# Kernel tuning notes

Hardware: AMD Instinct MI355X
Metric: run time of the kernel (lower is better)

The kernel has to match this reference:

```python
import jax, jax.numpy as jnp
import numpy as np

NL, H, PD, NH, NB = 4, 256, 64, 4, 65
B, L, AA = 2, 384, 48
DH = H // NH
MAX_REL = 32


def _ln(x, g, b):
    m = x.mean(-1, keepdims=True)
    v = ((x - m) ** 2).mean(-1, keepdims=True)
    return (x - m) * jax.lax.rsqrt(v + 1e-5) * g + b


def setup_inputs() -> dict:
    key = jax.random.key(0)
    ks = iter(jax.random.split(key, 64))
    w = lambda *s: jax.random.normal(next(ks), s, jnp.float32) * 0.02
    return dict(
        x=jax.random.normal(next(ks), (B, L, AA), jnp.float32),
        rp_w=w(AA, H), rp_b=jnp.zeros((H,), jnp.float32),
        pos_embed=w(L, H),
        pii_w=w(H, PD), pii_b=jnp.zeros((PD,), jnp.float32),
        pij_w=w(H, PD), pij_b=jnp.zeros((PD,), jnp.float32),
        rel_emb=w(2 * MAX_REL + 2, PD),
        ln_seq_g=jnp.ones((NL, H), jnp.float32), ln_seq_b=jnp.zeros((NL, H), jnp.float32),
        ln_pair_g=jnp.ones((NL, PD), jnp.float32), ln_pair_b=jnp.zeros((NL, PD), jnp.float32),
        pb_w=w(NL, PD, NH),
        in_w=w(NL, H, 3 * H), in_b=jnp.zeros((NL, 3 * H), jnp.float32),
        out_w=w(NL, H, H), out_b=jnp.zeros((NL, H), jnp.float32),
        ff_ln_g=jnp.ones((NL, H), jnp.float32), ff_ln_b=jnp.zeros((NL, H), jnp.float32),
        ff_w1=w(NL, H, 4 * H), ff_b1=jnp.zeros((NL, 4 * H), jnp.float32),
        ff_w2=w(NL, 4 * H, H), ff_b2=jnp.zeros((NL, H), jnp.float32),
        pu_ln_g=jnp.ones((NL, PD), jnp.float32), pu_ln_b=jnp.zeros((NL, PD), jnp.float32),
        pu_w1=w(NL, PD, PD), pu_b1=jnp.zeros((NL, PD), jnp.float32),
        pu_w2=w(NL, PD, PD), pu_b2=jnp.zeros((NL, PD), jnp.float32),
        outer_w=w(NL, 2 * H, PD), outer_b=jnp.zeros((NL, PD), jnp.float32),
        dh_ln_g=jnp.ones((PD,), jnp.float32), dh_ln_b=jnp.zeros((PD,), jnp.float32),
        dh_w1=w(PD, PD), dh_b1=jnp.zeros((PD,), jnp.float32),
        dh_w2=w(PD, NB), dh_b2=jnp.zeros((NB,), jnp.float32),
    )


def reference(x, rp_w, rp_b, pos_embed, pii_w, pii_b, pij_w, pij_b, rel_emb,
              ln_seq_g, ln_seq_b, ln_pair_g, ln_pair_b, pb_w, in_w, in_b,
              out_w, out_b, ff_ln_g, ff_ln_b, ff_w1, ff_b1, ff_w2, ff_b2,
              pu_ln_g, pu_ln_b, pu_w1, pu_b1, pu_w2, pu_b2, outer_w, outer_b,
              dh_ln_g, dh_ln_b, dh_w1, dh_b1, dh_w2, dh_b2):
    Bx, Lx, _ = x.shape
    gelu = lambda t: jax.nn.gelu(t, approximate=False)  # torch nn.GELU default (erf)
    h = x @ rp_w + rp_b + pos_embed[:Lx][None]
    # pair init: outer sum of two linear projections + clipped rel-pos embedding
    pair = (h @ pii_w + pii_b)[:, :, None, :] + (h @ pij_w + pij_b)[:, None, :, :]
    idx = jnp.arange(Lx)
    rel = jnp.clip(idx[None, :] - idx[:, None], -MAX_REL, MAX_REL) + MAX_REL  # (L,L)
    pair = pair + rel_emb[rel][None]
    for i in range(NL):
        seq_n = _ln(h, ln_seq_g[i], ln_seq_b[i])
        bias = _ln(pair, ln_pair_g[i], ln_pair_b[i]) @ pb_w[i]  # (B,L,L,NH)
        mask = bias.mean(axis=(0, 3))  # torch: permute->reshape(B*NH,L,L)->mean(0)
        qkv = seq_n @ in_w[i] + in_b[i]
        q, k, v = jnp.split(qkv, 3, axis=-1)
        q = q.reshape(Bx, Lx, NH, DH)
        k = k.reshape(Bx, Lx, NH, DH)
        v = v.reshape(Bx, Lx, NH, DH)
        scores = jnp.einsum('blhd,bmhd->bhlm', q, k) / float(np.sqrt(DH)) + mask
        attn = jax.nn.softmax(scores, axis=-1)
        o = jnp.einsum('bhlm,bmhd->blhd', attn, v).reshape(Bx, Lx, H)
        h = h + o @ out_w[i] + out_b[i]
        h = h + gelu(_ln(h, ff_ln_g[i], ff_ln_b[i]) @ ff_w1[i] + ff_b1[i]) @ ff_w2[i] + ff_b2[i]
        # outer_proj(cat([h_i, h_j])) == h@W[:H] outer-summed with h@W[H:]
        oi = h @ outer_w[i][:H]
        oj = h @ outer_w[i][H:]
        outer = oi[:, :, None, :] + oj[:, None, :, :] + outer_b[i]  # (B,L,L,PD)
        pair = pair + gelu(_ln(outer, pu_ln_g[i], pu_ln_b[i]) @ pu_w1[i] + pu_b1[i]) @ pu_w2[i] + pu_b2[i]
    logits = gelu(_ln(pair, dh_ln_g, dh_ln_b) @ dh_w1 + dh_b1) @ dh_w2 + dh_b2
    return (logits + jnp.swapaxes(logits, 1, 2)) / 2.0
```

## Files before the change

### kernel.cpp

```cpp
#include <hip/hip_runtime.h>
#include <math.h>

#define LSEQ 384
#define HD 256
#define PDIM 64
#define NHEAD 4
#define NBINS 65
#define BATCH 2
#define NTT (LSEQ / 16)
#define NTRI (NTT * (NTT + 1) / 2)

typedef __attribute__((ext_vector_type(8))) short bf16x8;
typedef __attribute__((ext_vector_type(16))) float f32x16;
typedef __attribute__((ext_vector_type(4))) float f32x4;
typedef __attribute__((ext_vector_type(4))) unsigned u32x4;
typedef __attribute__((ext_vector_type(4))) short s16x4;
#define MFMA32(a, b, c) __builtin_amdgcn_mfma_f32_32x32x16_bf16(a, b, c, 0, 0, 0)

template<int CTRL, int RMASK>
__device__ __forceinline__ float dpp_sum_step(float v) {
    int x = __builtin_amdgcn_update_dpp(0, __float_as_int(v), CTRL, RMASK, 0xf, true);
    return v + __int_as_float(x);
}
template<int CTRL, int RMASK>
// ... 81 lines not shown
                                        const unsigned short* __restrict__ srcB) {
    for (int idx = t; idx < 2048; idx += 256) {
        int rr2 = idx >> 5, cc2 = (idx & 31) * 2;
        *(unsigned*)&lw[0][rr2][cc2] = *(const unsigned*)(srcA + rr2 * 64 + cc2);
        *(unsigned*)&lw[1][rr2][cc2] = *(const unsigned*)(srcB + rr2 * 64 + cc2);
    }
}

__global__ void k_h_init(const float* __restrict__ x, const float* __restrict__ rp_w,
                         const float* __restrict__ rp_b, const float* __restrict__ pos,
                         float* __restrict__ h) {
    __shared__ float xs[48];
    int row = blockIdx.x;
    int l = row % LSEQ;
    int t = threadIdx.x;
    if (t < 48) xs[t] = x[row * 48 + t];
    __syncthreads();
    float acc = rp_b[t] + pos[l * HD + t];
#pragma unroll 8
    for (int a = 0; a < 48; ++a) acc += xs[a] * rp_w[a * HD + t];
    h[row * HD + t] = acc;
}

__global__ void k_proj2(const float* __restrict__ h, const float* __restrict__ wA,
                        const float* __restrict__ wB, const float* __restrict__ bA,
                        const float* __restrict__ bB, int center,
                        float* __restrict__ pA, float* __restrict__ pB) {
    __shared__ float hs[HD];
    int row = blockIdx.x;
    int t = threadIdx.x;
    hs[t] = h[row * HD + t];
    hs[t + 128] = h[row * HD + t + 128];
    __syncthreads();
    int col = t & 63;
    const float* w = (t < 64) ? wA : wB;
    const float* bias = (t < 64) ? bA : bB;
    float acc = bias ? bias[col] : 0.0f;
#pragma unroll 8
    for (int a = 0; a < HD; ++a) acc += hs[a] * w[a * PDIM + col];
    if (center) {
        float mean = wsum(acc) * (1.0f / PDIM);
        acc -= mean;
    }
    float* p = (t < 64) ? pA : pB;
    p[row * PDIM + col] = acc;
}

__global__ void __launch_bounds__(64) k_mask0(
    const float* __restrict__ pi, const float* __restrict__ pj,
    const float* __restrict__ rel_emb, const float* __restrict__ gpb,
    const float* __restrict__ cbv, float* __restrict__ mask_out) {
    __shared__ __align__(16) float pt[32][65];
    int blk = blockIdx.x;
    int row = blk / 12, seg = blk % 12;
    int b = row / LSEQ, i = row % LSEQ;
    int t = threadIdx.x;
    int pl = t & 31, hq = t >> 5;
    int j0 = seg * 32;
    float piv = pi[row * 64 + t];
    const float* pjb = pj + ((size_t)b * LSEQ + j0) * 64;
#pragma unroll 8
    for (int j = 0; j < 32; ++j) {
        int r = j0 + j - i; r = r < -32 ? -32 : (r > 32 ? 32 : r); r += 32;
        pt[j][t] = piv + pjb[j * 64 + t] + rel_emb[r * 64 + t];
    }
    __syncthreads();
    float vv[32];
    float sv = 0.0f;
#pragma unroll
    for (int c = 0; c < 32; ++c) { vv[c] = pt[pl][hq * 32 + c]; sv += vv[c]; }
    sv += __shfl_xor(sv, 32);
    float mean = sv * (1.0f / PDIM);
    float sd2 = 0.0f, sdg = 0.0f;
#pragma unroll
    for (int c = 0; c < 32; ++c) {
        float d = vv[c] - mean;
        sd2 = fmaf(d, d, sd2);
        sdg = fmaf(d, gpb[hq * 32 + c], sdg);
    }
    sd2 += __shfl_xor(sd2, 32);
    sdg += __shfl_xor(sdg, 32);
    float rsv = rsqrtf(sd2 * (1.0f / PDIM) + 1e-5f);
    float dot = rsv * sdg + cbv[0];
    if (hq == 0)
        atomicAdd(mask_out + i * LSEQ + j0 + pl, dot * (1.0f / (BATCH * NHEAD)));
}

__global__ void k_prep(const float* __restrict__ pu_ln_g, const float* __restrict__ pu_ln_b,
                       const float* __restrict__ pu_w1, const float* __restrict__ pu_b1,
                       const float* __restrict__ pu_w2,
                       const float* __restrict__ dh_ln_g, const float* __restrict__ dh_ln_b,
                       const float* __restrict__ dh_w1, const float* __restrict__ dh_b1,
                       const float* __restrict__ dh_w2,
                       unsigned short* __restrict__ w1hT, unsigned short* __restrict__ w1lT,
                       unsigned short* __restrict__ w2hT, unsigned short* __restrict__ w2lT,
                       float* __restrict__ b1p, float* __restrict__ w2c) {
    int i = blockIdx.x;
    int c = threadIdx.x;
    const float *g, *bb, *w1, *b1, *w2;
    int w2s;
    if (i < 4) { g = pu_ln_g + i * 64; bb = pu_ln_b + i * 64; w1 = pu_w1 + i * 4096;
                 b1 = pu_b1 + i * 64; w2 = pu_w2 + i * 4096; w2s = 64; }
    else       { g = dh_ln_g; bb = dh_ln_b; w1 = dh_w1; b1 = dh_b1; w2 = dh_w2; w2s = 65; }
    float accb = b1[c];
    for (int k = 0; k < 64; ++k) {
        float wv = w1[k * 64 + c];
        accb += bb[k] * wv;
        unsigned short h, l;
        split_bf(g[k] * wv, h, l);
        w1hT[i * 4096 + c * 64 + k] = h;
        w1lT[i * 4096 + c * 64 + k] = l;
        split_bf(w2[k * w2s + c], h, l);
        w2hT[i * 4096 + c * 64 + k] = h;
        w2lT[i * 4096 + c * 64 + k] = l;
    }
    b1p[i * 64 + c] = accb;
    if (i == 4) w2c[c] = dh_w2[c * 65 + 64];
}

__global__ void k_maskprep(const float* __restrict__ g, const float* __restrict__ bb,
                           const float* __restrict__ pbw, float* __restrict__ gp,
                           float* __restrict__ cb) {
    int li = blockIdx.x;
    int c = threadIdx.x;
    const float* pw = pbw + li * PDIM * NHEAD;
    float pbs = pw[c * 4] + pw[c * 4 + 1] + pw[c * 4 + 2] + pw[c * 4 + 3];
    gp[li * 64 + c] = g[li * 64 + c] * pbs;
    float s = wsum(bb[li * 64 + c] * pbs);
    if (c == 0) cb[li] = s;
}

__global__ void k_split_T(const float* __restrict__ src, unsigned short* __restrict__ dh,
                          unsigned short* __restrict__ dl, int K, int N,
                          int tiles_k, int tiles_n, size_t sstride, size_t dstride) {
    __shared__ float lds[64][65];
    int bid = blockIdx.x;
    int tpl = tiles_k * tiles_n;
    int layer = bid / tpl;
    int rest = bid % tpl;
    int kt = rest / tiles_n, nt = rest % tiles_n;
    const float* s = src + layer * sstride;
    int t = threadIdx.x, c = t & 63, r0 = t >> 6;
    for (int r = r0; r < 64; r += 4)
        lds[r][c] = s[(size_t)(kt * 64 + r) * N + nt * 64 + c];
    __syncthreads();
    unsigned short* oh = dh + layer * dstride;
    unsigned short* ol = dl + layer * dstride;
    for (int r = r0; r < 64; r += 4) {
        float v = lds[c][r];
        unsigned short h, l;
        split_bf(v, h, l);
        size_t o = (size_t)(nt * 64 + r) * K + kt * 64 + c;
        oh[o] = h;
        ol[o] = l;
    }
}

template<bool GELU>
__global__ void __launch_bounds__(64) k_gemm(
    const float* __restrict__ X, const unsigned short* __restrict__ wTh,
    const unsigned short* __restrict__ wTl, const float* __restrict__ bias,
    const float* __restrict__ R, float* __restrict__ OUT, int K, int N) {
    int idx = blockIdx.x;
    int lane = threadIdx.x & 63;
    int pl = lane & 31, hq = lane >> 5;
    int ntiles = N >> 5;
    int mt = idx / ntiles, nt = idx % ntiles;
    const float* xr = X + (size_t)(mt * 32 + pl) * K + 8 * hq;
    const unsigned short* bh = wTh + (size_t)(nt * 32 + pl) * K + 8 * hq;
    const unsigned short* bl = wTl + (size_t)(nt * 32 + pl) * K + 8 * hq;
    int n = nt * 32 + pl;
    float bv = bias[n];
    f32x16 acc;
#pragma unroll
    for (int r = 0; r < 16; ++r) {
        int mr = mt * 32 + (r & 3) + 8 * (r >> 2) + 4 * hq;
        acc[r] = bv + (R ? R[(size_t)mr * N + n] : 0.0f);
    }
#pragma unroll 4
    for (int s = 0; s < K; s += 16) {
        const f32x4* x4 = (const f32x4*)(xr + s);
        f32x4 xa = x4[0], xb = x4[1];
        float xv[8];
#pragma unroll
        for (int j = 0; j < 4; ++j) { xv[j] = xa[j]; xv[4 + j] = xb[j]; }
        u32x4 ah, al;
        pack8(xv, ah, al);
        bf16x8 bhv = *(const bf16x8*)(bh + s);
        bf16x8 blv = *(const bf16x8*)(bl + s);
        acc = MFMA32(as_bf(ah), bhv, acc);
        acc = MFMA32(as_bf(al), bhv, acc);
        acc = MFMA32(as_bf(ah), blv, acc);
    }
#pragma unroll
    for (int r = 0; r < 16; ++r) {
        int mr = mt * 32 + (r & 3) + 8 * (r >> 2) + 4 * hq;
        float v = acc[r];
        OUT[(size_t)mr * N + n] = GELU ? gelu_fast(v) : v;
    }
}

__global__ void k_ln_seq(const float* __restrict__ h, const float* __restrict__ g,
                         const float* __restrict__ b, float* __restrict__ out) {
    __shared__ float red[8];
    int row = blockIdx.x;
    int t = threadIdx.x;
    int w = t >> 6, lane = t & 63;
    float v = h[row * HD + t];
    float s = wsum(v);
    if (lane == 0) red[w] = s;
    __syncthreads();
    float mean = (red[0] + red[1] + red[2] + red[3]) * (1.0f / HD);
    float d = v - mean;
    float q = wsum(d * d);
    if (lane == 0) red[4 + w] = q;
    __syncthreads();
    float var = (red[4] + red[5] + red[6] + red[7]) * (1.0f / HD);
    out[row * HD + t] = d * rsqrtf(var + 1e-5f) * g[t] + b[t];
}

__global__ void k_attn(const float* __restrict__ qkv, const float* __restrict__ mask,
                       float* __restrict__ o) {
    __shared__ __align__(16) float qs[64];
    __shared__ float sc[LSEQ];
    __shared__ float red[8];
    __shared__ float op[4][64];
    int bid = blockIdx.x;
    int l = bid % LSEQ;
    int nh = (bid / LSEQ) & 3;
    int b = bid / (LSEQ * NHEAD);
    int t = threadIdx.x;
    int w = t >> 6, lane = t & 63;
    const float* qbase = qkv + ((size_t)(b * LSEQ + l)) * 768 + nh * 64;
    if (t < 64) qs[t] = qbase[t];
    __syncthreads();
    float lmax = -1e30f;
    float myv[2];
#pragma unroll
    for (int it = 0; it < 2; ++it) {
        int m = t + it * 256;
        if (m < LSEQ) {
            const float* kb = qkv + ((size_t)(b * LSEQ + m)) * 768 + 256 + nh * 64;
            const float4* k4 = (const float4*)kb;
            const float4* q4 = (const float4*)qs;
            float acc = 0.0f;
#pragma unroll
            for (int a = 0; a < 16; ++a) {
                float4 kv = k4[a], qv = q4[a];
                acc += qv.x * kv.x + qv.y * kv.y + qv.z * kv.z + qv.w * kv.w;
            }
            float s = acc * 0.125f + mask[l * LSEQ + m];
            myv[it] = s;
            lmax = fmaxf(lmax, s);
        } else myv[it] = -1e30f;
    }
    float wm = wmax(lmax);
    if (lane == 0) red[w] = wm;
    __syncthreads();
    float gmax = fmaxf(fmaxf(red[0], red[1]), fmaxf(red[2], red[3]));
    float lsum = 0.0f;
#pragma unroll
    for (int it = 0; it < 2; ++it) {
        int m = t + it * 256;
        if (m < LSEQ) {
            float e = expf(myv[it] - gmax);
            sc[m] = e;
            lsum += e;
        }
    }
    float ws = wsum(lsum);
    if (lane == 0) red[4 + w] = ws;
    __syncthreads();
    float inv = 1.0f / (red[4] + red[5] + red[6] + red[7]);
    int d = t & 63, gq = t >> 6;
    float part = 0.0f;
    for (int m = gq * 96; m < (gq + 1) * 96; ++m)
        part += sc[m] * qkv[((size_t)(b * LSEQ + m)) * 768 + 512 + nh * 64 + d];
    op[gq][d] = part;
    __syncthreads();
    if (t < 64) {
        float ov = (op[0][t] + op[1][t] + op[2][t] + op[3][t]) * inv;
        o[((size_t)(b * LSEQ + l)) * HD + nh * 64 + t] = ov;
    }
}

template<int MODE>
__global__ void __launch_bounds__(256, (MODE == 2) ? 2 : 3) k_pair_upd(
    const float* __restrict__ ojc,
    const float* __restrict__ oic,
    const unsigned short* __restrict__ w1hT, const unsigned short* __restrict__ w1lT,
    const float* __restrict__ b1p,
    const unsigned short* __restrict__ w2hT, const unsigned short* __restrict__ w2lT,
    const float* __restrict__ b2, float* __restrict__ pair,
    const float* __restrict__ gpb, const float* __restrict__ cbv,
    float* __restrict__ mask_out,
    const float* __restrict__ ipi, const float* __restrict__ ipj,
    const float* __restrict__ rel,
    const unsigned short* __restrict__ dw1h, const unsigned short* __restrict__ dw1l,
    const float* __restrict__ db1p,
    const unsigned short* __restrict__ dw2h, const unsigned short* __restrict__ dw2l,
    const float* __restrict__ w2c, const float* __restrict__ db2,
    float* __restrict__ outg) {
    constexpr bool DIST = (MODE == 2);
    __shared__ __align__(16) char smem[DIST ? 33344 : 17472];
    short (*lw)[64][68] = (short (*)[64][68])smem;
    int blk = blockIdx.x;
    int row = blk / 3, seg = blk % 3;
    int b = row / LSEQ;
    int t = threadIdx.x;
    int wave = t >> 6, lane = t & 63;
    int pl = lane & 31, hq = lane >> 5;
    int jj = wave * 32 + pl;
    int p = seg * 128 + jj;
    const float* ojr = ojc + ((size_t)b * LSEQ + p) * 64;
    const float* oir = oic + (size_t)row * 64;
    float* prp = pair + ((size_t)row * LSEQ + p) * 64;

    float v[32];
    {
        const f32x4* a4 = (const f32x4*)ojr;
        const f32x4* c4 = (const f32x4*)oir;
#pragma unroll
        for (int s = 0; s < 4; ++s) {
            f32x4 a = a4[4 * s + 2 * hq], aa = a4[4 * s + 2 * hq + 1];
            f32x4 c = c4[4 * s + 2 * hq], cc = c4[4 * s + 2 * hq + 1];
#pragma unroll
            for (int j = 0; j < 4; ++j) {
                v[8 * s + j] = a[j] + c[j];
                v[8 * s + 4 + j] = aa[j] + cc[j];
            }
        }
    }
    stage_w(lw, t, w1hT, w1lT);

    float ss = 0.0f;
#pragma unroll
    for (int i = 0; i < 32; ++i) ss = fmaf(v[i], v[i], ss);
    ss += __shfl_xor(ss, 32);
    float rs = rsqrtf(ss * (1.0f / PDIM) + 1e-5f);
#pragma unroll
    for (int i = 0; i < 32; ++i) v[i] *= rs;
    u32x4 zh[4], zl[4];
#pragma unroll
    for (int s = 0; s < 4; ++s) pack8(v + 8 * s, zh[s], zl[s]);

    const f32x4* b14 = (const f32x4*)b1p;
    f32x4 bi0[4], bi1[4];
#pragma unroll
    for (int g = 0; g < 4; ++g) { bi0[g] = b14[2 * g + hq]; bi1[g] = b14[8 + 2 * g + hq]; }

    __syncthreads();

    f32x16 acc0, acc1;
#pragma unroll
    for (int r = 0; r < 16; ++r) {
        acc0[r] = bi0[r >> 2][r & 3];
        acc1[r] = bi1[r >> 2][r & 3];
    }
#pragma unroll
    for (int s = 0; s < 4; ++s) {
        int ko = 16 * s + 8 * hq;
        bf16x8 a0h = ld8(&lw[0][pl][ko]);
        bf16x8 a0l = ld8(&lw[1][pl][ko]);
        bf16x8 a1h = ld8(&lw[0][32 + pl][ko]);
        bf16x8 a1l = ld8(&lw[1][32 + pl][ko]);
        bf16x8 zhs = as_bf(zh[s]), zls = as_bf(zl[s]);
        acc0 = MFMA32(a0h, zhs, acc0);
        acc0 = MFMA32(a0h, zls, acc0);
        acc0 = MFMA32(a0l, zhs, acc0);
        acc1 = MFMA32(a1h, zhs, acc1);
        acc1 = MFMA32(a1h, zls, acc1);
        acc1 = MFMA32(a1l, zhs, acc1);
    }
    __syncthreads();
    stage_w(lw, t, w2hT, w2lT);

    float u0[16], u1[16];
#pragma unroll
    for (int r = 0; r < 16; ++r) { u0[r] = gelu_erf(acc0[r]); u1[r] = gelu_erf(acc1[r]); }

    f32x4 r0[4], r1[4], q0[4], q1[4];
    {
        const f32x4* b24 = (const f32x4*)b2;
        if constexpr (MODE == 0) {
            int l = row % LSEQ;
            int rr_ = p - l; rr_ = rr_ < -32 ? -32 : (rr_ > 32 ? 32 : rr_); rr_ += 32;
            const f32x4* i4 = (const f32x4*)(ipi + (size_t)row * 64);
            const f32x4* j4 = (const f32x4*)(ipj + ((size_t)b * LSEQ + p) * 64);
            const f32x4* e4 = (const f32x4*)(rel + rr_ * 64);
#pragma unroll
            for (int g = 0; g < 4; ++g) {
                r0[g] = i4[2 * g + hq] + j4[2 * g + hq] + e4[2 * g + hq];
                r1[g] = i4[8 + 2 * g + hq] + j4[8 + 2 * g + hq] + e4[8 + 2 * g + hq];
                q0[g] = b24[2 * g + hq];
                q1[g] = b24[8 + 2 * g + hq];
            }
        } else {
            const f32x4* pr4 = (const f32x4*)prp;
#pragma unroll
            for (int g = 0; g < 4; ++g) {
                r0[g] = pr4[2 * g + hq];
                r1[g] = pr4[8 + 2 * g + hq];
                q0[g] = b24[2 * g + hq];
                q1[g] = b24[8 + 2 * g + hq];
            }
        }
    }

    float rA0[4], rB0[4], rA1[4], rB1[4];
#pragma unroll
    for (int i = 0; i < 4; ++i) {
        rA0[i] = __shfl_xor(hq ? u0[i] : u0[4 + i], 32);
        rB0[i] = __shfl_xor(hq ? u0[8 + i] : u0[12 + i], 32);
        rA1[i] = __shfl_xor(hq ? u1[i] : u1[4 + i], 32);
        rB1[i] = __shfl_xor(hq ? u1[8 + i] : u1[12 + i], 32);
    }
    u32x4 uh[4], ul[4];
#pragma unroll
    for (int s = 0; s < 4; ++s) {
        int tt = s >> 1, q = s & 1;
        float fg[8];
#pragma unroll
        for (int i = 0; i < 4; ++i) {
            float own_f = q ? (tt ? u1[8 + i] : u0[8 + i]) : (tt ? u1[i] : u0[i]);
            float own_s = q ? (tt ? u1[12 + i] : u0[12 + i]) : (tt ? u1[4 + i] : u0[4 + i]);
            float rcv   = q ? (tt ? rB1[i] : rB0[i]) : (tt ? rA1[i] : rA0[i]);
            fg[i]     = hq ? rcv : own_f;
            fg[4 + i] = hq ? own_s : rcv;
        }
        pack8(fg, uh[s], ul[s]);
    }

    __syncthreads();

    f32x16 c0, c1;
#pragma unroll
    for (int r = 0; r < 16; ++r) {
        int g = r >> 2, i = r & 3;
        c0[r] = q0[g][i] + r0[g][i];
        c1[r] = q1[g][i] + r1[g][i];
    }
#pragma unroll
    for (int s = 0; s < 4; ++s) {
        int ko = 16 * s + 8 * hq;
        bf16x8 a0h = ld8(&lw[0][pl][ko]);
        bf16x8 a0l = ld8(&lw[1][pl][ko]);
        bf16x8 a1h = ld8(&lw[0][32 + pl][ko]);
        bf16x8 a1l = ld8(&lw[1][32 + pl][ko]);
        bf16x8 uhs = as_bf(uh[s]), uls = as_bf(ul[s]);
        c0 = MFMA32(a0h, uhs, c0);
        c0 = MFMA32(a0h, uls, c0);
        c0 = MFMA32(a0l, uhs, c0);
        c1 = MFMA32(a1h, uhs, c1);
        c1 = MFMA32(a1h, uls, c1);
        c1 = MFMA32(a1l, uhs, c1);
    }

    if constexpr (!DIST) {
        const f32x4* gp4 = (const f32x4*)gpb;
        f32x4 gp0[4], gp1[4];
#pragma unroll
        for (int g = 0; g < 4; ++g) { gp0[g] = gp4[2 * g + hq]; gp1[g] = gp4[8 + 2 * g + hq]; }
        float sv = 0.0f;
#pragma unroll
        for (int r = 0; r < 16; ++r) sv += c0[r] + c1[r];
        sv += __shfl_xor(sv, 32);
        float mean = sv * (1.0f / PDIM);
        float sd2 = 0.0f, sdg = 0.0f;
#pragma unroll 4
        for (int r = 0; r < 16; ++r) {
            int g = r >> 2, i = r & 3;
            float d0 = c0[r] - mean, d1 = c1[r] - mean;
            sd2 = fmaf(d0, d0, sd2);
            sd2 = fmaf(d1, d1, sd2);
            sdg = fmaf(d0, gp0[g][i], sdg);
            sdg = fmaf(d1, gp1[g][i], sdg);
        }
        sd2 += __shfl_xor(sd2, 32);
        sdg += __shfl_xor(sdg, 32);
        float rsv = rsqrtf(sd2 * (1.0f / PDIM) + 1e-5f);
        float dot = rsv * sdg + cbv[0];
        if (hq == 0)
            atomicAdd(mask_out + (row % LSEQ) * LSEQ + p, dot * (1.0f / (BATCH * NHEAD)));
        f32x4* pw4 = (f32x4*)prp;
#pragma unroll
        for (int g = 0; g < 4; ++g) {
            f32x4 s0, s1;
#pragma unroll
            for (int i = 0; i < 4; ++i) { s0[i] = c0[4 * g + i]; s1[i] = c1[4 * g + i]; }
            pw4[2 * g + hq] = s0;
            pw4[8 + 2 * g + hq] = s1;
        }
    } else {
        float ra[4], rb[4], rc[4], rd[4];
#pragma unroll
        for (int i = 0; i < 4; ++i) {
            ra[i] = __shfl_xor(hq ? c0[i] : c0[4 + i], 32);
            rb[i] = __shfl_xor(hq ? c0[8 + i] : c0[12 + i], 32);
            rc[i] = __shfl_xor(hq ? c1[i] : c1[4 + i], 32);
            rd[i] = __shfl_xor(hq ? c1[8 + i] : c1[12 + i], 32);
        }
        float v2[32];
#pragma unroll
        for (int i = 0; i < 4; ++i) {
            v2[i]      = hq ? ra[i] : c0[i];
            v2[4 + i]  = hq ? c0[4 + i] : ra[i];
            v2[8 + i]  = hq ? rb[i] : c0[8 + i];
            v2[12 + i] = hq ? c0[12 + i] : rb[i];
            v2[16 + i] = hq ? rc[i] : c1[i];
            v2[20 + i] = hq ? c1[4 + i] : rc[i];
            v2[24 + i] = hq ? rd[i] : c1[8 + i];
            v2[28 + i] = hq ? c1[12 + i] : rd[i];
        }
        __syncthreads();
        stage_w(lw, t, dw1h, dw1l);

        float sm = 0.0f;
#pragma unroll
        for (int i = 0; i < 32; ++i) sm += v2[i];
        sm += __shfl_xor(sm, 32);
        float mean = sm * (1.0f / PDIM);
        float ss2 = 0.0f;
#pragma unroll
        for (int i = 0; i < 32; ++i) { v2[i] -= mean; ss2 = fmaf(v2[i], v2[i], ss2); }
        ss2 += __shfl_xor(ss2, 32);
        float rs2 = rsqrtf(ss2 * (1.0f / PDIM) + 1e-5f);
#pragma unroll
        for (int i = 0; i < 32; ++i) v2[i] *= rs2;
#pragma unroll
        for (int s = 0; s < 4; ++s) pack8(v2 + 8 * s, zh[s], zl[s]);

        const f32x4* d14 = (const f32x4*)db1p;
        const f32x4* d24 = (const f32x4*)db2;
        const f32x4* wc4 = (const f32x4*)w2c;
        f32x4 di0[4], di1[4], e0[4], e1[4], wc0[4], wc1[4];
#pragma unroll
        for (int g = 0; g < 4; ++g) {
            di0[g] = d14[2 * g + hq]; di1[g] = d14[8 + 2 * g + hq];
            e0[g] = d24[2 * g + hq];  e1[g] = d24[8 + 2 * g + hq];
            wc0[g] = wc4[2 * g + hq]; wc1[g] = wc4[8 + 2 * g + hq];
        }
        __syncthreads();

#pragma unroll
        for (int r = 0; r < 16; ++r) {
            acc0[r] = di0[r >> 2][r & 3];
            acc1[r] = di1[r >> 2][r & 3];
        }
#pragma unroll
        for (int s = 0; s < 4; ++s) {
            int ko = 16 * s + 8 * hq;
            bf16x8 a0h = ld8(&lw[0][pl][ko]);
            bf16x8 a0l = ld8(&lw[1][pl][ko]);
            bf16x8 a1h = ld8(&lw[0][32 + pl][ko]);
            bf16x8 a1l = ld8(&lw[1][32 + pl][ko]);
            bf16x8 zhs = as_bf(zh[s]), zls = as_bf(zl[s]);
            acc0 = MFMA32(a0h, zhs, acc0);
            acc0 = MFMA32(a0h, zls, acc0);
            acc0 = MFMA32(a0l, zhs, acc0);
            acc1 = MFMA32(a1h, zhs, acc1);
            acc1 = MFMA32(a1h, zls, acc1);
            acc1 = MFMA32(a1l, zhs, acc1);
        }
        __syncthreads();
        stage_w(lw, t, dw2h, dw2l);

        float p64 = 0.0f;
#pragma unroll
        for (int r = 0; r < 16; ++r) {
            int g = r >> 2, i = r & 3;
            u0[r] = gelu_erf(acc0[r]);
            u1[r] = gelu_erf(acc1[r]);
            p64 = fmaf(u0[r], wc0[g][i], p64);
            p64 = fmaf(u1[r], wc1[g][i], p64);
        }
        p64 += __shfl_xor(p64, 32);
#pragma unroll
        for (int i = 0; i < 4; ++i) {
            rA0[i] = __shfl_xor(hq ? u0[i] : u0[4 + i], 32);
            rB0[i] = __shfl_xor(hq ? u0[8 + i] : u0[12 + i], 32);
            rA1[i] = __shfl_xor(hq ? u1[i] : u1[4 + i], 32);
            rB1[i] = __shfl_xor(hq ? u1[8 + i] : u1[12 + i], 32);
        }
#pragma unroll
        for (int s = 0; s < 4; ++s) {
            int tt = s >> 1, q = s & 1;
            float fg[8];
#pragma unroll
            for (int i = 0; i < 4; ++i) {
                float own_f = q ? (tt ? u1[8 + i] : u0[8 + i]) : (tt ? u1[i] : u0[i]);
                float own_s = q ? (tt ? u1[12 + i] : u0[12 + i]) : (tt ? u1[4 + i] : u0[4 + i]);
                float rcv   = q ? (tt ? rB1[i] : rB0[i]) : (tt ? rA1[i] : rA0[i]);
                fg[i]     = hq ? rcv : own_f;
                fg[4 + i] = hq ? own_s : rcv;
            }
            pack8(fg, uh[s], ul[s]);
        }
        __syncthreads();

#pragma unroll
        for (int r = 0; r < 16; ++r) {
            c0[r] = e0[r >> 2][r & 3];
            c1[r] = e1[r >> 2][r & 3];
        }
#pragma unroll
        for (int s = 0; s < 4; ++s) {
            int ko = 16 * s + 8 * hq;
            bf16x8 a0h = ld8(&lw[0][pl][ko]);
            bf16x8 a0l = ld8(&lw[1][pl][ko]);
            bf16x8 a1h = ld8(&lw[0][32 + pl][ko]);
            bf16x8 a1l = ld8(&lw[1][32 + pl][ko]);
            bf16x8 uhs = as_bf(uh[s]), uls = as_bf(ul[s]);
            c0 = MFMA32(a0h, uhs, c0);
            c0 = MFMA32(a0h, uls, c0);
            c0 = MFMA32(a0l, uhs, c0);
            c1 = MFMA32(a1h, uhs, c1);
            c1 = MFMA32(a1h, uls, c1);
            c1 = MFMA32(a1l, uhs, c1);
        }
        __syncthreads();
        float (*pt)[65] = (float (*)[65])smem;
#pragma unroll
        for (int r = 0; r < 16; ++r) {
            int rr = (r & 3) + 8 * (r >> 2) + 4 * hq;
            pt[jj][rr] = c0[r];
            pt[jj][32 + rr] = c1[r];
        }
        if (hq == 0) pt[jj][64] = p64 + db2[64];
        __syncthreads();
        float4* dst = (float4*)(outg + ((size_t)row * LSEQ + seg * 128) * NBINS);
        const float4* srcl = (const float4*)&pt[0][0];
        for (int n = t; n < 128 * NBINS / 4; n += 256) dst[n] = srcl[n];
    }
}

__global__ void k_sym(float* __restrict__ out) {
    int u = blockIdx.x;
    int b = 0;
    if (u >= NTRI) { b = 1; u -= NTRI; }
    int lt = 0, rem = NTT;
    while (u >= rem) { u -= rem; ++lt; --rem; }
    int mt = lt + u;
    int t = threadIdx.x;
    int g = t >> 6, lane = t & 63;
    float* ob = out + (size_t)b * LSEQ * LSEQ * NBINS;
    for (int e = g; e < 256; e += 4) {
        int i = e >> 4, j = e & 15;
        if (lt == mt && j < i) continue;
        size_t ia = ((size_t)(lt * 16 + i) * LSEQ + (mt * 16 + j)) * NBINS;
        size_t ib = ((size_t)(mt * 16 + j) * LSEQ + (lt * 16 + i)) * NBINS;
        for (int k = lane; k < NBINS; k += 64) {
            float a = ob[ia + k], c = ob[ib + k];
            float vv = 0.5f * (a + c);
            ob[ia + k] = vv;
            if (ia != ib) ob[ib + k] = vv;
        }
    }
}

extern "C" void kernel_launch(void* const* d_in, const int* in_sizes, int n_in,
                              void* d_out, int out_size, void* d_ws, size_t ws_size,
                              hipStream_t stream) {
    const float* x        = (const float*)d_in[0];
    const float* rp_w     = (const float*)d_in[1];
    const float* rp_b     = (const float*)d_in[2];
    const float* pos      = (const float*)d_in[3];
    const float* pii_w    = (const float*)d_in[4];
    const float* pii_b    = (const float*)d_in[5];
    const float* pij_w    = (const float*)d_in[6];
    const float* pij_b    = (const float*)d_in[7];
    const float* rel_emb  = (const float*)d_in[8];
    const float* ln_seq_g = (const float*)d_in[9];
    const float* ln_seq_b = (const float*)d_in[10];
    const float* ln_pair_g= (const float*)d_in[11];
    const float* ln_pair_b= (const float*)d_in[12];
    const float* pb_w     = (const float*)d_in[13];
    const float* in_w     = (const float*)d_in[14];
    const float* in_b     = (const float*)d_in[15];
    const float* out_w    = (const float*)d_in[16];
    const float* out_b    = (const float*)d_in[17];
    const float* ff_ln_g  = (const float*)d_in[18];
    const float* ff_ln_b  = (const float*)d_in[19];
    const float* ff_w1    = (const float*)d_in[20];
    const float* ff_b1    = (const float*)d_in[21];
    const float* ff_w2    = (const float*)d_in[22];
    const float* ff_b2    = (const float*)d_in[23];
    const float* pu_ln_g  = (const float*)d_in[24];
    const float* pu_ln_b  = (const float*)d_in[25];
    const float* pu_w1    = (const float*)d_in[26];
    const float* pu_b1    = (const float*)d_in[27];
    const float* pu_w2    = (const float*)d_in[28];
    const float* pu_b2    = (const float*)d_in[29];
    const float* outer_w  = (const float*)d_in[30];
    const float* outer_b  = (const float*)d_in[31];
    const float* dh_ln_g  = (const float*)d_in[32];
    const float* dh_ln_b  = (const float*)d_in[33];
    const float* dh_w1    = (const float*)d_in[34];
    const float* dh_b1    = (const float*)d_in[35];
    const float* dh_w2    = (const float*)d_in[36];
    const float* dh_b2    = (const float*)d_in[37];
    float* outp = (float*)d_out;

    float* W = (float*)d_ws;
    float* h    = W;  W += BATCH * LSEQ * HD;
    float* sn   = W;  W += BATCH * LSEQ * HD;
    float* qkv  = W;  W += BATCH * LSEQ * 3 * HD;
    float* ob   = W;  W += BATCH * LSEQ * HD;
    float* mid  = W;  W += BATCH * LSEQ * 4 * HD;
    float* maskA= W;  W += LSEQ * LSEQ;
    float* maskB= W;  W += LSEQ * LSEQ;
    float* poi  = W;  W += BATCH * LSEQ * PDIM;
    float* poj  = W;  W += BATCH * LSEQ * PDIM;
    float* poi0 = W;  W += BATCH * LSEQ * PDIM;
    float* poj0 = W;  W += BATCH * LSEQ * PDIM;
    float* b1p  = W;  W += 5 * 64;
    float* w2c  = W;  W += 64;
    float* gpb  = W;  W += 4 * 64;
    float* cbv  = W;  W += 64;
    unsigned short* w1hT = (unsigned short*)W;  W += 5 * 2048;
    unsigned short* w1lT = (unsigned short*)W;  W += 5 * 2048;
    unsigned short* w2hT = (unsigned short*)W;  W += 5 * 2048;
    unsigned short* w2lT = (unsigned short*)W;  W += 5 * 2048;
    unsigned short* qwT_h = (unsigned short*)W;  W += 4 * 196608 / 2;
    unsigned short* qwT_l = (unsigned short*)W;  W += 4 * 196608 / 2;
    unsigned short* owT_h = (unsigned short*)W;  W += 4 * 65536 / 2;
    unsigned short* owT_l = (unsigned short*)W;  W += 4 * 65536 / 2;
    unsigned short* f1T_h = (unsigned short*)W;  W += 4 * 262144 / 2;
    unsigned short* f1T_l = (unsigned short*)W;  W += 4 * 262144 / 2;
    unsigned short* f2T_h = (unsigned short*)W;  W += 4 * 262144 / 2;
    unsigned short* f2T_l = (unsigned short*)W;  W += 4 * 262144 / 2;
    float* pair = W;  W += (size_t)BATCH * LSEQ * LSEQ * PDIM;

    const int rows = BATCH * LSEQ;

    k_prep<<<5, 64, 0, stream>>>(pu_ln_g, pu_ln_b, pu_w1, pu_b1, pu_w2,
                                 dh_ln_g, dh_ln_b, dh_w1, dh_b1, dh_w2,
                                 w1hT, w1lT, w2hT, w2lT, b1p, w2c);
    k_maskprep<<<4, 64, 0, stream>>>(ln_pair_g, ln_pair_b, pb_w, gpb, cbv);
    k_split_T<<<4 * 4 * 12, 256, 0, stream>>>(in_w,  qwT_h, qwT_l, 256, 768,  4, 12, 196608, 196608);
    k_split_T<<<4 * 4 * 4,  256, 0, stream>>>(out_w, owT_h, owT_l, 256, 256,  4, 4,  65536,  65536);
    k_split_T<<<4 * 4 * 16, 256, 0, stream>>>(ff_w1, f1T_h, f1T_l, 256, 1024, 4, 16, 262144, 262144);
    k_split_T<<<4 * 16 * 4, 256, 0, stream>>>(ff_w2, f2T_h, f2T_l, 1024, 256, 16, 4, 262144, 262144);
    k_h_init<<<rows, 256, 0, stream>>>(x, rp_w, rp_b, pos, h);
    k_proj2<<<rows, 128, 0, stream>>>(h, pii_w, pij_w, pii_b, pij_b, 0, poi0, poj0);
    hipMemsetAsync(maskA, 0, LSEQ * LSEQ * sizeof(float), stream);
    k_mask0<<<rows * 12, 64, 0, stream>>>(poi0, poj0, rel_emb, gpb, cbv, maskA);

    float* mcur = maskA;
    float* mnext = maskB;
    for (int i = 0; i < 4; ++i) {
        k_ln_seq<<<rows, 256, 0, stream>>>(h, ln_seq_g + i * HD, ln_seq_b + i * HD, sn);
        k_gemm<false><<<576, 64, 0, stream>>>(sn, qwT_h + i * 196608, qwT_l + i * 196608,
                                              in_b + i * 768, nullptr, qkv, 256, 768);
        k_attn<<<BATCH * NHEAD * LSEQ, 256, 0, stream>>>(qkv, mcur, ob);
        k_gemm<false><<<192, 64, 0, stream>>>(ob, owT_h + i * 65536, owT_l + i * 65536,
                                              out_b + i * 256, h, h, 256, 256);
        k_ln_seq<<<rows, 256, 0, stream>>>(h, ff_ln_g + i * HD, ff_ln_b + i * HD, sn);
        k_gemm<true><<<768, 64, 0, stream>>>(sn, f1T_h + i * 262144, f1T_l + i * 262144,
                                             ff_b1 + i * 1024, nullptr, mid, 256, 1024);
        k_gemm<false><<<192, 64, 0, stream>>>(mid, f2T_h + i * 262144, f2T_l + i * 262144,
                                              ff_b2 + i * 256, h, h, 1024, 256);
        k_proj2<<<rows, 128, 0, stream>>>(h, outer_w + i * 2 * HD * PDIM,
                                          outer_w + i * 2 * HD * PDIM + HD * PDIM,
                                          outer_b + i * PDIM, nullptr, 1, poi, poj);
        if (i == 0) {
            hipMemsetAsync(mnext, 0, LSEQ * LSEQ * sizeof(float), stream);
            k_pair_upd<0><<<rows * 3, 256, 0, stream>>>(
                poj, poi,
                w1hT, w1lT, b1p, w2hT, w2lT, pu_b2, pair,
                gpb + 64, cbv + 1, mnext, poi0, poj0, rel_emb,
                nullptr, nullptr, nullptr, nullptr, nullptr, nullptr, nullptr, nullptr);
            float* tmp = mcur; mcur = mnext; mnext = tmp;
        } else if (i < 3) {
            hipMemsetAsync(mnext, 0, LSEQ * LSEQ * sizeof(float), stream);
            k_pair_upd<1><<<rows * 3, 256, 0, stream>>>(
                poj, poi,
                w1hT + i * 4096, w1lT + i * 4096, b1p + i * 64,
                w2hT + i * 4096, w2lT + i * 4096, pu_b2 + i * PDIM, pair,
                gpb + (i + 1) * 64, cbv + (i + 1), mnext,
                nullptr, nullptr, nullptr,
                nullptr, nullptr, nullptr, nullptr, nullptr, nullptr, nullptr, nullptr);
            float* tmp = mcur; mcur = mnext; mnext = tmp;
        } else {
            k_pair_upd<2><<<rows * 3, 256, 0, stream>>>(
                poj, poi,
                w1hT + 3 * 4096, w1lT + 3 * 4096, b1p + 3 * 64,
                w2hT + 3 * 4096, w2lT + 3 * 4096, pu_b2 + 3 * PDIM, pair,
                nullptr, nullptr, nullptr,
                nullptr, nullptr, nullptr,
                w1hT + 4 * 4096, w1lT + 4 * 4096, b1p + 4 * 64,
                w2hT + 4 * 4096, w2lT + 4 * 4096, w2c, dh_b2, outp);
        }
    }

    k_sym<<<2 * NTRI, 256, 0, stream>>>(outp);
}
```

Baseline: 1.025 ms.

## Process full pair row per block with both MLP weights staged once

For the non-final pair-update modes, each block now handles a whole row (three 128-column segments in a loop) instead of one segment. Both weight matrices are staged into shared memory once, in separate buffers, before the loop. This removes the repeated weight staging and the intra-block syncs between the two GEMMs. In exchange the grid is one third the size and shared memory per block doubles, which may lower occupancy and parallelism.

```diff
diff --git a/kernel.cpp b/kernel.cpp
--- a/kernel.cpp
+++ b/kernel.cpp
@@ -407,100 +407,271 @@
     const float* __restrict__ w2c, const float* __restrict__ db2,
     float* __restrict__ outg) {
     constexpr bool DIST = (MODE == 2);
-    __shared__ __align__(16) char smem[DIST ? 33344 : 17472];
-    short (*lw)[64][68] = (short (*)[64][68])smem;
-    int blk = blockIdx.x;
-    int row = blk / 3, seg = blk % 3;
-    int b = row / LSEQ;
+    __shared__ __align__(16) char smem[DIST ? 33344 : 34816];
     int t = threadIdx.x;
     int wave = t >> 6, lane = t & 63;
     int pl = lane & 31, hq = lane >> 5;
     int jj = wave * 32 + pl;
-    int p = seg * 128 + jj;
-    const float* ojr = ojc + ((size_t)b * LSEQ + p) * 64;
-    const float* oir = oic + (size_t)row * 64;
-    float* prp = pair + ((size_t)row * LSEQ + p) * 64;
-
-    float v[32];
-    {
-        const f32x4* a4 = (const f32x4*)ojr;
-        const f32x4* c4 = (const f32x4*)oir;
+
+    if constexpr (!DIST) {
+        short (*lw1)[64][68] = (short (*)[64][68])smem;
+        short (*lw2)[64][68] = (short (*)[64][68])(smem + 17408);
+        int row = blockIdx.x;
+        int b = row / LSEQ;
+        int l = row % LSEQ;
+        const float* oir = oic + (size_t)row * 64;
+        stage_w(lw1, t, w1hT, w1lT);
+        stage_w(lw2, t, w2hT, w2lT);
+        __syncthreads();
+
+        for (int seg = 0; seg < 3; ++seg) {
+            int p = seg * 128 + jj;
+            const float* ojr = ojc + ((size_t)b * LSEQ + p) * 64;
+            float* prp = pair + ((size_t)row * LSEQ + p) * 64;
+
+            float v[32];
+            {
+                const f32x4* a4 = (const f32x4*)ojr;
+                const f32x4* c4 = (const f32x4*)oir;
+#pragma unroll
+                for (int s = 0; s < 4; ++s) {
+                    f32x4 a = a4[4 * s + 2 * hq], aa = a4[4 * s + 2 * hq + 1];
+                    f32x4 c = c4[4 * s + 2 * hq], cc = c4[4 * s + 2 * hq + 1];
+#pragma unroll
+                    for (int j = 0; j < 4; ++j) {
+                        v[8 * s + j] = a[j] + c[j];
+                        v[8 * s + 4 + j] = aa[j] + cc[j];
+                    }
+                }
+            }
+            float ss = 0.0f;
+#pragma unroll
+            for (int i = 0; i < 32; ++i) ss = fmaf(v[i], v[i], ss);
+            ss += __shfl_xor(ss, 32);
+            float rs = rsqrtf(ss * (1.0f / PDIM) + 1e-5f);
+#pragma unroll
+            for (int i = 0; i < 32; ++i) v[i] *= rs;
+            u32x4 zh[4], zl[4];
+#pragma unroll
+            for (int s = 0; s < 4; ++s) pack8(v + 8 * s, zh[s], zl[s]);
+
+            const f32x4* b14 = (const f32x4*)b1p;
+            f32x16 acc0, acc1;
+#pragma unroll
+            for (int g = 0; g < 4; ++g) {
+                f32x4 bb0 = b14[2 * g + hq], bb1 = b14[8 + 2 * g + hq];
+#pragma unroll
+                for (int i = 0; i < 4; ++i) {
+                    acc0[4 * g + i] = bb0[i];
+                    acc1[4 * g + i] = bb1[i];
+                }
+            }
+#pragma unroll
+            for (int s = 0; s < 4; ++s) {
+                int ko = 16 * s + 8 * hq;
+                bf16x8 a0h = ld8(&lw1[0][pl][ko]);
+                bf16x8 a0l = ld8(&lw1[1][pl][ko]);
+                bf16x8 a1h = ld8(&lw1[0][32 + pl][ko]);
+                bf16x8 a1l = ld8(&lw1[1][32 + pl][ko]);
+                bf16x8 zhs = as_bf(zh[s]), zls = as_bf(zl[s]);
+                acc0 = MFMA32(a0h, zhs, acc0);
+                acc0 = MFMA32(a0h, zls, acc0);
+                acc0 = MFMA32(a0l, zhs, acc0);
+                acc1 = MFMA32(a1h, zhs, acc1);
+                acc1 = MFMA32(a1h, zls, acc1);
+                acc1 = MFMA32(a1l, zhs, acc1);
+            }
+            float u0[16], u1[16];
+#pragma unroll
+            for (int r = 0; r < 16; ++r) { u0[r] = gelu_erf(acc0[r]); u1[r] = gelu_erf(acc1[r]); }
+
+            f32x4 r0[4], r1[4], q0[4], q1[4];
+            {
+                const f32x4* b24 = (const f32x4*)b2;
+                if constexpr (MODE == 0) {
+                    int rr_ = p - l; rr_ = rr_ < -32 ? -32 : (rr_ > 32 ? 32 : rr_); rr_ += 32;
+                    const f32x4* i4 = (const f32x4*)(ipi + (size_t)row * 64);
+                    const f32x4* j4 = (const f32x4*)(ipj + ((size_t)b * LSEQ + p) * 64);
+                    const f32x4* e4 = (const f32x4*)(rel + rr_ * 64);
+#pragma unroll
+                    for (int g = 0; g < 4; ++g) {
+                        r0[g] = i4[2 * g + hq] + j4[2 * g + hq] + e4[2 * g + hq];
+                        r1[g] = i4[8 + 2 * g + hq] + j4[8 + 2 * g + hq] + e4[8 + 2 * g + hq];
+                        q0[g] = b24[2 * g + hq];
+                        q1[g] = b24[8 + 2 * g + hq];
+                    }
+                } else {
+                    const f32x4* pr4 = (const f32x4*)prp;
+#pragma unroll
+                    for (int g = 0; g < 4; ++g) {
+                        r0[g] = pr4[2 * g + hq];
+                        r1[g] = pr4[8 + 2 * g + hq];
+                        q0[g] = b24[2 * g + hq];
+                        q1[g] = b24[8 + 2 * g + hq];
+                    }
+                }
+            }
+
+            float rA0[4], rB0[4], rA1[4], rB1[4];
+#pragma unroll
+            for (int i = 0; i < 4; ++i) {
+                rA0[i] = __shfl_xor(hq ? u0[i] : u0[4 + i], 32);
+                rB0[i] = __shfl_xor(hq ? u0[8 + i] : u0[12 + i], 32);
+                rA1[i] = __shfl_xor(hq ? u1[i] : u1[4 + i], 32);
+                rB1[i] = __shfl_xor(hq ? u1[8 + i] : u1[12 + i], 32);
+            }
+            u32x4 uh[4], ul[4];
+#pragma unroll
+            for (int s = 0; s < 4; ++s) {
+                int tt = s >> 1, q = s & 1;
+                float fg[8];
+#pragma unroll
+                for (int i = 0; i < 4; ++i) {
+                    float own_f = q ? (tt ? u1[8 + i] : u0[8 + i]) : (tt ? u1[i] : u0[i]);
+                    float own_s = q ? (tt ? u1[12 + i] : u0[12 + i]) : (tt ? u1[4 + i] : u0[4 + i]);
+                    float rcv   = q ? (tt ? rB1[i] : rB0[i]) : (tt ? rA1[i] : rA0[i]);
+                    fg[i]     = hq ? rcv : own_f;
+                    fg[4 + i] = hq ? own_s : rcv;
+                }
+                pack8(fg, uh[s], ul[s]);
+            }
+
+            f32x16 c0, c1;
+#pragma unroll
+            for (int r = 0; r < 16; ++r) {
+                int g = r >> 2, i = r & 3;
+                c0[r] = q0[g][i] + r0[g][i];
+                c1[r] = q1[g][i] + r1[g][i];
+            }
+#pragma unroll
+            for (int s = 0; s < 4; ++s) {
+                int ko = 16 * s + 8 * hq;
+                bf16x8 a0h = ld8(&lw2[0][pl][ko]);
+                bf16x8 a0l = ld8(&lw2[1][pl][ko]);
+                bf16x8 a1h = ld8(&lw2[0][32 + pl][ko]);
+                bf16x8 a1l = ld8(&lw2[1][32 + pl][ko]);
+                bf16x8 uhs = as_bf(uh[s]), uls = as_bf(ul[s]);
+                c0 = MFMA32(a0h, uhs, c0);
+                c0 = MFMA32(a0h, uls, c0);
+                c0 = MFMA32(a0l, uhs, c0);
+                c1 = MFMA32(a1h, uhs, c1);
+                c1 = MFMA32(a1h, uls, c1);
+                c1 = MFMA32(a1l, uhs, c1);
+            }
+
+            {
+                const f32x4* gp4 = (const f32x4*)gpb;
+                f32x4 gp0[4], gp1[4];
+#pragma unroll
+                for (int g = 0; g < 4; ++g) { gp0[g] = gp4[2 * g + hq]; gp1[g] = gp4[8 + 2 * g + hq]; }
+                float sv = 0.0f;
+#pragma unroll
+                for (int r = 0; r < 16; ++r) sv += c0[r] + c1[r];
+                sv += __shfl_xor(sv, 32);
+                float mean = sv * (1.0f / PDIM);
+                float sd2 = 0.0f, sdg = 0.0f;
+#pragma unroll 4
+                for (int r = 0; r < 16; ++r) {
+                    int g = r >> 2, i = r & 3;
+                    float d0 = c0[r] - mean, d1 = c1[r] - mean;
+                    sd2 = fmaf(d0, d0, sd2);
+                    sd2 = fmaf(d1, d1, sd2);
+                    sdg = fmaf(d0, gp0[g][i], sdg);
+                    sdg = fmaf(d1, gp1[g][i], sdg);
+                }
+                sd2 += __shfl_xor(sd2, 32);
+                sdg += __shfl_xor(sdg, 32);
+                float rsv = rsqrtf(sd2 * (1.0f / PDIM) + 1e-5f);
+                float dot = rsv * sdg + cbv[0];
+                if (hq == 0)
+                    atomicAdd(mask_out + l * LSEQ + p, dot * (1.0f / (BATCH * NHEAD)));
+            }
+            f32x4* pw4 = (f32x4*)prp;
+#pragma unroll
+            for (int g = 0; g < 4; ++g) {
+                f32x4 s0, s1;
+#pragma unroll
+                for (int i = 0; i < 4; ++i) { s0[i] = c0[4 * g + i]; s1[i] = c1[4 * g + i]; }
+                pw4[2 * g + hq] = s0;
+                pw4[8 + 2 * g + hq] = s1;
+            }
+        }
+    } else {
+        short (*lw)[64][68] = (short (*)[64][68])smem;
+        int blk = blockIdx.x;
+        int row = blk / 3, seg = blk % 3;
+        int b = row / LSEQ;
+        int p = seg * 128 + jj;
+        const float* ojr = ojc + ((size_t)b * LSEQ + p) * 64;
+        const float* oir = oic + (size_t)row * 64;
+        float* prp = pair + ((size_t)row * LSEQ + p) * 64;
+
+        float v[32];
+        {
+            const f32x4* a4 = (const f32x4*)ojr;
+            const f32x4* c4 = (const f32x4*)oir;
+#pragma unroll
+            for (int s = 0; s < 4; ++s) {
+                f32x4 a = a4[4 * s + 2 * hq], aa = a4[4 * s + 2 * hq + 1];
+                f32x4 c = c4[4 * s + 2 * hq], cc = c4[4 * s + 2 * hq + 1];
+#pragma unroll
+                for (int j = 0; j < 4; ++j) {
+                    v[8 * s + j] = a[j] + c[j];
+                    v[8 * s + 4 + j] = aa[j] + cc[j];
+                }
+            }
+        }
+        stage_w(lw, t, w1hT, w1lT);
+
+        float ss = 0.0f;
+#pragma unroll
+        for (int i = 0; i < 32; ++i) ss = fmaf(v[i], v[i], ss);
+        ss += __shfl_xor(ss, 32);
+        float rs = rsqrtf(ss * (1.0f / PDIM) + 1e-5f);
+#pragma unroll
+        for (int i = 0; i < 32; ++i) v[i] *= rs;
+        u32x4 zh[4], zl[4];
+#pragma unroll
+        for (int s = 0; s < 4; ++s) pack8(v + 8 * s, zh[s], zl[s]);
+
+        const f32x4* b14 = (const f32x4*)b1p;
+        f32x4 bi0[4], bi1[4];
+#pragma unroll
+        for (int g = 0; g < 4; ++g) { bi0[g] = b14[2 * g + hq]; bi1[g] = b14[8 + 2 * g + hq]; }
+
+        __syncthreads();
+
+        f32x16 acc0, acc1;
+#pragma unroll
+        for (int r = 0; r < 16; ++r) {
+            acc0[r] = bi0[r >> 2][r & 3];
+            acc1[r] = bi1[r >> 2][r & 3];
+        }
 #pragma unroll
         for (int s = 0; s < 4; ++s) {
-            f32x4 a = a4[4 * s + 2 * hq], aa = a4[4 * s + 2 * hq + 1];
-            f32x4 c = c4[4 * s + 2 * hq], cc = c4[4 * s + 2 * hq + 1];
-#pragma unroll
-            for (int j = 0; j < 4; ++j) {
-                v[8 * s + j] = a[j] + c[j];
-                v[8 * s + 4 + j] = aa[j] + cc[j];
-            }
-        }
-    }
-    stage_w(lw, t, w1hT, w1lT);
-
-    float ss = 0.0f;
-#pragma unroll
-    for (int i = 0; i < 32; ++i) ss = fmaf(v[i], v[i], ss);
-    ss += __shfl_xor(ss, 32);
-    float rs = rsqrtf(ss * (1.0f / PDIM) + 1e-5f);
-#pragma unroll
-    for (int i = 0; i < 32; ++i) v[i] *= rs;
-    u32x4 zh[4], zl[4];
-#pragma unroll
-    for (int s = 0; s < 4; ++s) pack8(v + 8 * s, zh[s], zl[s]);
-
-    const f32x4* b14 = (const f32x4*)b1p;
-    f32x4 bi0[4], bi1[4];
-#pragma unroll
-    for (int g = 0; g < 4; ++g) { bi0[g] = b14[2 * g + hq]; bi1[g] = b14[8 + 2 * g + hq]; }
-
-    __syncthreads();
-
-    f32x16 acc0, acc1;
-#pragma unroll
-    for (int r = 0; r < 16; ++r) {
-        acc0[r] = bi0[r >> 2][r & 3];
-        acc1[r] = bi1[r >> 2][r & 3];
-    }
-#pragma unroll
-    for (int s = 0; s < 4; ++s) {
-        int ko = 16 * s + 8 * hq;
-        bf16x8 a0h = ld8(&lw[0][pl][ko]);
-        bf16x8 a0l = ld8(&lw[1][pl][ko]);
-        bf16x8 a1h = ld8(&lw[0][32 + pl][ko]);
-        bf16x8 a1l = ld8(&lw[1][32 + pl][ko]);
-        bf16x8 zhs = as_bf(zh[s]), zls = as_bf(zl[s]);
-        acc0 = MFMA32(a0h, zhs, acc0);
-        acc0 = MFMA32(a0h, zls, acc0);
-        acc0 = MFMA32(a0l, zhs, acc0);
-        acc1 = MFMA32(a1h, zhs, acc1);
-        acc1 = MFMA32(a1h, zls, acc1);
-        acc1 = MFMA32(a1l, zhs, acc1);
-    }
-    __syncthreads();
-    stage_w(lw, t, w2hT, w2lT);
-
-    float u0[16], u1[16];
-#pragma unroll
-    for (int r = 0; r < 16; ++r) { u0[r] = gelu_erf(acc0[r]); u1[r] = gelu_erf(acc1[r]); }
-
-    f32x4 r0[4], r1[4], q0[4], q1[4];
-    {
-        const f32x4* b24 = (const f32x4*)b2;
-        if constexpr (MODE == 0) {
-            int l = row % LSEQ;
-            int rr_ = p - l; rr_ = rr_ < -32 ? -32 : (rr_ > 32 ? 32 : rr_); rr_ += 32;
-            const f32x4* i4 = (const f32x4*)(ipi + (size_t)row * 64);
-            const f32x4* j4 = (const f32x4*)(ipj + ((size_t)b * LSEQ + p) * 64);
-            const f32x4* e4 = (const f32x4*)(rel + rr_ * 64);
-#pragma unroll
-            for (int g = 0; g < 4; ++g) {
-                r0[g] = i4[2 * g + hq] + j4[2 * g + hq] + e4[2 * g + hq];
-                r1[g] = i4[8 + 2 * g + hq] + j4[8 + 2 * g + hq] + e4[8 + 2 * g + hq];
-                q0[g] = b24[2 * g + hq];
-                q1[g] = b24[8 + 2 * g + hq];
-            }
-        } else {
+            int ko = 16 * s + 8 * hq;
+            bf16x8 a0h = ld8(&lw[0][pl][ko]);
+            bf16x8 a0l = ld8(&lw[1][pl][ko]);
+            bf16x8 a1h = ld8(&lw[0][32 + pl][ko]);
+            bf16x8 a1l = ld8(&lw[1][32 + pl][ko]);
+            bf16x8 zhs = as_bf(zh[s]), zls = as_bf(zl[s]);
+            acc0 = MFMA32(a0h, zhs, acc0);
+            acc0 = MFMA32(a0h, zls, acc0);
+            acc0 = MFMA32(a0l, zhs, acc0);
+            acc1 = MFMA32(a1h, zhs, acc1);
+            acc1 = MFMA32(a1h, zls, acc1);
+            acc1 = MFMA32(a1l, zhs, acc1);
+        }
+        __syncthreads();
+        stage_w(lw, t, w2hT, w2lT);
+
+        float u0[16], u1[16];
+#pragma unroll
+        for (int r = 0; r < 16; ++r) { u0[r] = gelu_erf(acc0[r]); u1[r] = gelu_erf(acc1[r]); }
+
+        f32x4 r0[4], r1[4], q0[4], q1[4];
+        {
+            const f32x4* b24 = (const f32x4*)b2;
             const f32x4* pr4 = (const f32x4*)prp;
 #pragma unroll
             for (int g = 0; g < 4; ++g) {
@@ -510,93 +681,56 @@
                 q1[g] = b24[8 + 2 * g + hq];
             }
         }
-    }
-
-    float rA0[4], rB0[4], rA1[4], rB1[4];
-#pragma unroll
-    for (int i = 0; i < 4; ++i) {
-        rA0[i] = __shfl_xor(hq ? u0[i] : u0[4 + i], 32);
-        rB0[i] = __shfl_xor(hq ? u0[8 + i] : u0[12 + i], 32);
-        rA1[i] = __shfl_xor(hq ? u1[i] : u1[4 + i], 32);
-        rB1[i] = __shfl_xor(hq ? u1[8 + i] : u1[12 + i], 32);
-    }
-    u32x4 uh[4], ul[4];
-#pragma unroll
-    for (int s = 0; s < 4; ++s) {
-        int tt = s >> 1, q = s & 1;
-        float fg[8];
+
+        float rA0[4], rB0[4], rA1[4], rB1[4];
 #pragma unroll
         for (int i = 0; i < 4; ++i) {
-            float own_f = q ? (tt ? u1[8 + i] : u0[8 + i]) : (tt ? u1[i] : u0[i]);
-            float own_s = q ? (tt ? u1[12 + i] : u0[12 + i]) : (tt ? u1[4 + i] : u0[4 + i]);
-            float rcv   = q ? (tt ? rB1[i] : rB0[i]) : (tt ? rA1[i] : rA0[i]);
-            fg[i]     = hq ? rcv : own_f;
-            fg[4 + i] = hq ? own_s : rcv;
-        }
-        pack8(fg, uh[s], ul[s]);
-    }
-
-    __syncthreads();
-
-    f32x16 c0, c1;
-#pragma unroll
-    for (int r = 0; r < 16; ++r) {
-        int g = r >> 2, i = r & 3;
-        c0[r] = q0[g][i] + r0[g][i];
-        c1[r] = q1[g][i] + r1[g][i];
-    }
-#pragma unroll
-    for (int s = 0; s < 4; ++s) {
-        int ko = 16 * s + 8 * hq;
-        bf16x8 a0h = ld8(&lw[0][pl][ko]);
-        bf16x8 a0l = ld8(&lw[1][pl][ko]);
-        bf16x8 a1h = ld8(&lw[0][32 + pl][ko]);
-        bf16x8 a1l = ld8(&lw[1][32 + pl][ko]);
-        bf16x8 uhs = as_bf(uh[s]), uls = as_bf(ul[s]);
-        c0 = MFMA32(a0h, uhs, c0);
-        c0 = MFMA32(a0h, uls, c0);
-        c0 = MFMA32(a0l, uhs, c0);
-        c1 = MFMA32(a1h, uhs, c1);
-        c1 = MFMA32(a1h, uls, c1);
-        c1 = MFMA32(a1l, uhs, c1);
-    }
-
-    if constexpr (!DIST) {
-        const f32x4* gp4 = (const f32x4*)gpb;
-        f32x4 gp0[4], gp1[4];
-#pragma unroll
-        for (int g = 0; g < 4; ++g) { gp0[g] = gp4[2 * g + hq]; gp1[g] = gp4[8 + 2 * g + hq]; }
-        float sv = 0.0f;
-#pragma unroll
-        for (int r = 0; r < 16; ++r) sv += c0[r] + c1[r];
-        sv += __shfl_xor(sv, 32);
-        float mean = sv * (1.0f / PDIM);
-        float sd2 = 0.0f, sdg = 0.0f;
-#pragma unroll 4
+            rA0[i] = __shfl_xor(hq ? u0[i] : u0[4 + i], 32);
+            rB0[i] = __shfl_xor(hq ? u0[8 + i] : u0[12 + i], 32);
+            rA1[i] = __shfl_xor(hq ? u1[i] : u1[4 + i], 32);
+            rB1[i] = __shfl_xor(hq ? u1[8 + i] : u1[12 + i], 32);
+        }
+        u32x4 uh[4], ul[4];
+#pragma unroll
+        for (int s = 0; s < 4; ++s) {
+            int tt = s >> 1, q = s & 1;
+            float fg[8];
+#pragma unroll
+            for (int i = 0; i < 4; ++i) {
+                float own_f = q ? (tt ? u1[8 + i] : u0[8 + i]) : (tt ? u1[i] : u0[i]);
+                float own_s = q ? (tt ? u1[12 + i] : u0[12 + i]) : (tt ? u1[4 + i] : u0[4 + i]);
+                float rcv   = q ? (tt ? rB1[i] : rB0[i]) : (tt ? rA1[i] : rA0[i]);
+                fg[i]     = hq ? rcv : own_f;
+                fg[4 + i] = hq ? own_s : rcv;
+            }
+            pack8(fg, uh[s], ul[s]);
+        }
+
+        __syncthreads();
+
+        f32x16 c0, c1;
+#pragma unroll
         for (int r = 0; r < 16; ++r) {
             int g = r >> 2, i = r & 3;
-            float d0 = c0[r] - mean, d1 = c1[r] - mean;
-            sd2 = fmaf(d0, d0, sd2);
-            sd2 = fmaf(d1, d1, sd2);
-            sdg = fmaf(d0, gp0[g][i], sdg);
-            sdg = fmaf(d1, gp1[g][i], sdg);
-        }
-        sd2 += __shfl_xor(sd2, 32);
-        sdg += __shfl_xor(sdg, 32);
-        float rsv = rsqrtf(sd2 * (1.0f / PDIM) + 1e-5f);
-        float dot = rsv * sdg + cbv[0];
-        if (hq == 0)
-            atomicAdd(mask_out + (row % LSEQ) * LSEQ + p, dot * (1.0f / (BATCH * NHEAD)));
-        f32x4* pw4 = (f32x4*)prp;
-#pragma unroll
-        for (int g = 0; g < 4; ++g) {
-            f32x4 s0, s1;
-#pragma unroll
-            for (int i = 0; i < 4; ++i) { s0[i] = c0[4 * g + i]; s1[i] = c1[4 * g + i]; }
-            pw4[2 * g + hq] = s0;
-            pw4[8 + 2 * g + hq] = s1;
-        }
-    } else {
+            c0[r] = q0[g][i] + r0[g][i];
+            c1[r] = q1[g][i] + r1[g][i];
+        }
+#pragma unroll
+        for (int s = 0; s < 4; ++s) {
+            int ko = 16 * s + 8 * hq;
+            bf16x8 a0h = ld8(&lw[0][pl][ko]);
+            bf16x8 a0l = ld8(&lw[1][pl][ko]);
+            bf16x8 a1h = ld8(&lw[0][32 + pl][ko]);
+            bf16x8 a1l = ld8(&lw[1][32 + pl][ko]);
+            bf16x8 uhs = as_bf(uh[s]), uls = as_bf(ul[s]);
+            c0 = MFMA32(a0h, uhs, c0);
+            c0 = MFMA32(a0h, uls, c0);
+            c0 = MFMA32(a0l, uhs, c0);
+            c1 = MFMA32(a1h, uhs, c1);
+            c1 = MFMA32(a1h, uls, c1);
+            c1 = MFMA32(a1l, uhs, c1);
+        }
+
         float ra[4], rb[4], rc[4], rd[4];
 #pragma unroll
         for (int i = 0; i < 4; ++i) {
@@ -870,7 +1004,7 @@
                                           outer_b + i * PDIM, nullptr, 1, poi, poj);
         if (i == 0) {
             hipMemsetAsync(mnext, 0, LSEQ * LSEQ * sizeof(float), stream);
-            k_pair_upd<0><<<rows * 3, 256, 0, stream>>>(
+            k_pair_upd<0><<<rows, 256, 0, stream>>>(
                 poj, poi,
                 w1hT, w1lT, b1p, w2hT, w2lT, pu_b2, pair,
                 gpb + 64, cbv + 1, mnext, poi0, poj0, rel_emb,
@@ -878,7 +1012,7 @@
             float* tmp = mcur; mcur = mnext; mnext = tmp;
         } else if (i < 3) {
             hipMemsetAsync(mnext, 0, LSEQ * LSEQ * sizeof(float), stream);
-            k_pair_upd<1><<<rows * 3, 256, 0, stream>>>(
+            k_pair_upd<1><<<rows, 256, 0, stream>>>(
                 poj, poi,
                 w1hT + i * 4096, w1lT + i * 4096, b1p + i * 64,
                 w2hT + i * 4096, w2lT + i * 4096, pu_b2 + i * PDIM, pair,
```

New measurement: 1.101 ms. 7.4% more time.
